# Optimization experiments

Hardware: AMD Instinct MI355X
Metric: run time of the kernel (lower is better)

The kernel has to match this reference:

```python
import jax, jax.numpy as jnp
import numpy as np

EPS = 1e-5
N_HEAD = 8
D_MODEL = 1024
D_K = D_MODEL // N_HEAD


def setup_inputs() -> dict:
    key = jax.random.key(0)
    ks = jax.random.split(key, 6)
    B, N = 4, 8192
    scale = 0.02
    return {
        "query": jax.random.normal(ks[0], (B, N, D_MODEL), jnp.float32),
        "key": jax.random.normal(ks[1], (B, N, D_MODEL), jnp.float32),
        "value": jax.random.normal(ks[2], (B, N, D_MODEL), jnp.float32),
        "Wq": jax.random.normal(ks[3], (D_MODEL, D_MODEL), jnp.float32) * scale,
        "bq": jnp.zeros((D_MODEL,), jnp.float32),
        "Wk": jax.random.normal(ks[4], (D_MODEL, D_MODEL), jnp.float32) * scale,
        "bk": jnp.zeros((D_MODEL,), jnp.float32),
        "Wv": jax.random.normal(ks[5], (D_MODEL, D_MODEL), jnp.float32) * scale,
        "bv": jnp.zeros((D_MODEL,), jnp.float32),
        "gamma_K": jnp.ones((N_HEAD, D_K), jnp.float32),
        "beta_K": jnp.zeros((N_HEAD, D_K), jnp.float32),
        "gamma_V": jnp.ones((N_HEAD, D_K), jnp.float32),
        "beta_V": jnp.zeros((N_HEAD, D_K), jnp.float32),
    }


def _proj_heads(x, W, b):
    # x: [B,N,D], torch Linear: x @ W.T + b -> [B,H,N,d_k]
    B, N, _ = x.shape
    y = jnp.einsum('bnd,ed->bne', x, W) + b
    return y.reshape(B, N, N_HEAD, D_K).transpose(0, 2, 1, 3)


def _layernorm_per_head(x, gamma, beta):
    # x: [B,H,N,d_k]; gamma/beta: [H,d_k] broadcast over batch and seq
    mu = jnp.mean(x, axis=-1, keepdims=True)
    var = jnp.mean((x - mu) ** 2, axis=-1, keepdims=True)
    xn = (x - mu) * jax.lax.rsqrt(var + EPS)
    return xn * gamma[None, :, None, :] + beta[None, :, None, :]


def reference(query, key, value, Wq, bq, Wk, bk, Wv, bv,
              gamma_K, beta_K, gamma_V, beta_V):
    B, N, _ = query.shape
    q = _proj_heads(query, Wq, bq)   # [B,H,N,dk]
    k = _proj_heads(key, Wk, bk)
    v = _proj_heads(value, Wv, bv)
    # galerkin: layernorm on K and V per head
    k = _layernorm_per_head(k, gamma_K, beta_K)
    v = _layernorm_per_head(v, gamma_V, beta_V)
    # linear attention: (K^T V)/N then Q @ (.)
    scores = jnp.einsum('bhnd,bhne->bhde', k, v)  # [B,H,dk,dk]
    p_attn = scores / N
    x = jnp.einsum('bhnd,bhde->bhne', q, p_attn)  # [B,H,N,dk]
    att_output = x.transpose(0, 2, 1, 3).reshape(B, N, N_HEAD * D_K)
    return (att_output, p_attn)
```

## Files before the change

kernel.cpp:

```cpp
#include <hip/hip_runtime.h>
#include <stdint.h>

#define DM 1024
#define NHEAD 8
#define DK 128
#define BATCH 4
#define SEQ 8192
#define ROWS (BATCH*SEQ)
#define EPSL 1e-5f
#define NSPLIT 8

typedef __attribute__((ext_vector_type(8)))  short    bf16x8;
typedef __attribute__((ext_vector_type(4)))  short    short4v;
typedef __attribute__((ext_vector_type(4)))  float    f32x4;
typedef __attribute__((ext_vector_type(4)))  float    float4v;
typedef __attribute__((ext_vector_type(2)))  uint32_t uint2v;
typedef __attribute__((ext_vector_type(4)))  uint32_t uint4v;

union AFrag { bf16x8 v; short4v h[2]; int i4[4]; };
union U8    { uint4v v[2]; uint32_t u[8]; };

__device__ inline uint32_t pack2bf(float a, float b){
  uint32_t ua = __builtin_bit_cast(uint32_t, a) + 0x8000u;
  uint32_t ub = __builtin_bit_cast(uint32_t, b) + 0x8000u;
  return (ua >> 16) | (ub & 0xffff0000u);
}

__global__ void wconv_kernel(const float* __restrict__ src, uint32_t* __restrict__ dst, int n8){
  int i = blockIdx.x*256 + threadIdx.x;
  if (i >= n8) return;
  const float4v* s = (const float4v*)src;
  float4v v0 = s[2*i], v1 = s[2*i+1];
  uint4v o;
  o.x = pack2bf(v0.x, v0.y); o.y = pack2bf(v0.z, v0.w);
  o.z = pack2bf(v1.x, v1.y); o.w = pack2bf(v1.z, v1.w);
  ((uint4v*)dst)[i] = o;
}

template<int MODE>
__global__ __launch_bounds__(256, 2)
void gemm_core(const float* __restrict__ A, const uint16_t* __restrict__ Bw,
               const float* __restrict__ bias, const float* __restrict__ gamma,
               const float* __restrict__ beta, uint16_t* __restrict__ outb,
               float* __restrict__ outf)
{
  __shared__ uint16_t As[128][36];
  __shared__ uint16_t Bs[128][36];
  __shared__ float red_s[2][128];
  __shared__ float red_q[2][128];

  const int tid = threadIdx.x;
  const int id  = blockIdx.x;
  const int xcd = id & 7, j = id >> 3;
  const int bM  = ((j >> 3) << 3) | xcd;
  const int bN  = j & 7;
  const int lane = tid & 63, wv = tid >> 6;
  const int wm = wv & 1, wn = wv >> 1;
  const int l15 = lane & 15, l4 = lane >> 4;

  const int sr = tid >> 1, sh = tid & 1;
  const float* Ap = A + (size_t)(bM*128 + sr)*DM + sh*16;
  const uint16_t* Bbase = Bw + (MODE==1 ? (size_t)(bM>>6)*1048576 : (size_t)0);
  const uint16_t* Bp = Bbase + (size_t)(bN*128 + sr)*DM + sh*16;
  uint32_t* asw = (uint32_t*)&As[sr][sh*16];
  uint32_t* bsw = (uint32_t*)&Bs[sr][sh*16];

  f32x4 acc[4][4];
  #pragma unroll
  for (int i=0;i<4;i++)
    #pragma unroll
    for (int jj=0;jj<4;jj++) acc[i][jj] = (f32x4)(0.0f);

  const uint16_t* Ard = &As[wm*64 + l15][l4*8];
  const uint16_t* Brd = &Bs[wn*64 + l15][l4*8];

  float4v a0 = *(const float4v*)(Ap);
  float4v a1 = *(const float4v*)(Ap+4);
  float4v a2 = *(const float4v*)(Ap+8);
  float4v a3 = *(const float4v*)(Ap+12);
  uint4v  b0 = *(const uint4v*)(Bp);
  uint4v  b1 = *(const uint4v*)(Bp+8);
  Ap += 32; Bp += 32;

  for (int k0 = 0; k0 < DM; k0 += 32){
    uint32_t p0 = pack2bf(a0.x,a0.y), p1 = pack2bf(a0.z,a0.w);
    uint32_t p2 = pack2bf(a1.x,a1.y), p3 = pack2bf(a1.z,a1.w);
    uint32_t p4 = pack2bf(a2.x,a2.y), p5 = pack2bf(a2.z,a2.w);
    uint32_t p6 = pack2bf(a3.x,a3.y), p7 = pack2bf(a3.z,a3.w);
    uint4v  c0 = b0, c1 = b1;
    __syncthreads();
    { uint2v t; t.x=p0;   t.y=p1;   ((uint2v*)asw)[0]=t; }
    { uint2v t; t.x=p2;   t.y=p3;   ((uint2v*)asw)[1]=t; }
    { uint2v t; t.x=p4;   t.y=p5;   ((uint2v*)asw)[2]=t; }
    { uint2v t; t.x=p6;   t.y=p7;   ((uint2v*)asw)[3]=t; }
    { uint2v t; t.x=c0.x; t.y=c0.y; ((uint2v*)bsw)[0]=t; }
    { uint2v t; t.x=c0.z; t.y=c0.w; ((uint2v*)bsw)[1]=t; }
    { uint2v t; t.x=c1.x; t.y=c1.y; ((uint2v*)bsw)[2]=t; }
    { uint2v t; t.x=c1.z; t.y=c1.w; ((uint2v*)bsw)[3]=t; }
    __syncthreads();

    if (k0 + 32 < DM){
      a0 = *(const float4v*)(Ap);
      a1 = *(const float4v*)(Ap+4);
      a2 = *(const float4v*)(Ap+8);
      a3 = *(const float4v*)(Ap+12);
      b0 = *(const uint4v*)(Bp);
      b1 = *(const uint4v*)(Bp+8);
      Ap += 32; Bp += 32;
    }

    AFrag af[4], bf4[4];
    #pragma unroll
    for (int mt=0; mt<4; mt++){
      af[mt].h[0] = *(const short4v*)(Ard + mt*16*36);
      af[mt].h[1] = *(const short4v*)(Ard + mt*16*36 + 4);
    }
    #pragma unroll
    for (int nt=0; nt<4; nt++){
      bf4[nt].h[0] = *(const short4v*)(Brd + nt*16*36);
      bf4[nt].h[1] = *(const short4v*)(Brd + nt*16*36 + 4);
    }
    #pragma unroll
    for (int mt=0; mt<4; mt++)
      #pragma unroll
      for (int nt=0; nt<4; nt++)
        acc[mt][nt] = __builtin_amdgcn_mfma_f32_16x16x32_bf16(af[mt].v, bf4[nt].v, acc[mt][nt], 0, 0, 0);
  }

  if (MODE == 0){
    float bv[4], gv[4], btv[4];
    #pragma unroll
    for (int nt=0; nt<4; nt++){
      int col = bN*128 + wn*64 + nt*16 + l15;
      bv[nt] = bias[col]; gv[nt] = gamma[col]; btv[nt] = beta[col];
    }
    #pragma unroll
    for (int mt=0; mt<4; mt++){
      #pragma unroll
      for (int i=0; i<4; i++){
        float sm = 0.f, sq = 0.f;
        #pragma unroll
        for (int nt=0; nt<4; nt++){
          float v = acc[mt][nt][i] + bv[nt];
          acc[mt][nt][i] = v;
          sm += v; sq += v*v;
        }
        #pragma unroll
        for (int off=1; off<16; off<<=1){
          sm += __shfl_xor(sm, off, 16);
          sq += __shfl_xor(sq, off, 16);
        }
        if (l15 == 0){
          int rl = wm*64 + mt*16 + l4*4 + i;
          red_s[wn][rl] = sm; red_q[wn][rl] = sq;
        }
      }
    }
    __syncthreads();
    #pragma unroll
    for (int mt=0; mt<4; mt++){
      #pragma unroll
      for (int i=0; i<4; i++){
        int rl = wm*64 + mt*16 + l4*4 + i;
        float sum = red_s[0][rl] + red_s[1][rl];
        float ssq = red_q[0][rl] + red_q[1][rl];
        float mean = sum * (1.f/DK);
        float var  = ssq * (1.f/DK) - mean*mean;
        float rs   = rsqrtf(var + EPSL);
        size_t row = (size_t)(bM*128 + rl);
        #pragma unroll
        for (int nt=0; nt<4; nt++){
          int col = bN*128 + wn*64 + nt*16 + l15;
          float o = (acc[mt][nt][i] - mean)*rs*gv[nt] + btv[nt];
          uint32_t u = __builtin_bit_cast(uint32_t, o) + 0x8000u;
          outb[row*DM + col] = (uint16_t)(u >> 16);
        }
      }
    }
  } else {
    const int bb = bM >> 6;
    float bv[4];
    #pragma unroll
    for (int nt=0; nt<4; nt++)
      bv[nt] = bias[bb*DM + bN*128 + wn*64 + nt*16 + l15];
    #pragma unroll
    for (int mt=0; mt<4; mt++){
      #pragma unroll
      for (int i=0; i<4; i++){
        size_t row = (size_t)(bM*128 + wm*64 + mt*16 + l4*4 + i);
        #pragma unroll
        for (int nt=0; nt<4; nt++){
          int col = bN*128 + wn*64 + nt*16 + l15;
          outf[row*DM + col] = acc[mt][nt][i] + bv[nt];
        }
      }
    }
  }
}

__global__ __launch_bounds__(256, 2)
void scores_kernel(const uint16_t* __restrict__ kln, const uint16_t* __restrict__ vln,
                   float* __restrict__ part)
{
  __shared__ uint16_t kT[128][70];
  __shared__ uint16_t vT[128][70];
  const int tid = threadIdx.x;
  const int sp = blockIdx.x & 7, bh = blockIdx.x >> 3;
  const int b = bh >> 3, h = bh & 7;
  const int lane = tid & 63, wv = tid >> 6, wm = wv & 1, wn = wv >> 1;
  const int l15 = lane & 15, l4 = lane >> 4;
  const int dg = tid & 7, np = tid >> 3;

  f32x4 acc[4][4];
  #pragma unroll
  for (int i=0;i<4;i++)
    #pragma unroll
    for (int jj=0;jj<4;jj++) acc[i][jj] = (f32x4)(0.0f);

  const size_t hb = (size_t)b*SEQ*DM + (size_t)h*DK;

  auto load_slab = [&](int nc, U8& k0, U8& k1, U8& v0, U8& v1){
    const int n0 = sp*1024 + nc*64;
    const uint16_t* kp = kln + hb + (size_t)(n0 + 2*np)*DM + dg*16;
    const uint16_t* vp = vln + hb + (size_t)(n0 + 2*np)*DM + dg*16;
    k0.v[0] = *(const uint4v*)(kp);       k0.v[1] = *(const uint4v*)(kp+8);
    k1.v[0] = *(const uint4v*)(kp+DM);    k1.v[1] = *(const uint4v*)(kp+DM+8);
    v0.v[0] = *(const uint4v*)(vp);       v0.v[1] = *(const uint4v*)(vp+8);
    v1.v[0] = *(const uint4v*)(vp+DM);    v1.v[1] = *(const uint4v*)(vp+DM+8);
  };

  U8 k0, k1, v0, v1;
  load_slab(0, k0, k1, v0, v1);

  for (int nc = 0; nc < 16; nc++){
    __syncthreads();
    #pragma unroll
    for (int q=0; q<8; q++){
      uint32_t ke = (k0.u[q] & 0xffffu) | (k1.u[q] << 16);
      uint32_t ko = (k0.u[q] >> 16)     | (k1.u[q] & 0xffff0000u);
      uint32_t ve = (v0.u[q] & 0xffffu) | (v1.u[q] << 16);
      uint32_t vo = (v0.u[q] >> 16)     | (v1.u[q] & 0xffff0000u);
      int d = dg*16 + q*2;
      *(uint32_t*)&kT[d  ][2*np] = ke;
      *(uint32_t*)&kT[d+1][2*np] = ko;
      *(uint32_t*)&vT[d  ][2*np] = ve;
      *(uint32_t*)&vT[d+1][2*np] = vo;
    }
    __syncthreads();

    if (nc + 1 < 16) load_slab(nc + 1, k0, k1, v0, v1);

    #pragma unroll
    for (int ks=0; ks<2; ks++){
      const int koff = ks*32 + l4*8;
      AFrag af[4], bf4[4];
      #pragma unroll
      for (int mt=0; mt<4; mt++){
        const uint16_t* pr = &kT[wm*64 + mt*16 + l15][koff];
        af[mt].i4[0] = *(const int*)(pr);
        af[mt].i4[1] = *(const int*)(pr+2);
        af[mt].i4[2] = *(const int*)(pr+4);
        af[mt].i4[3] = *(const int*)(pr+6);
      }
      #pragma unroll
      for (int nt=0; nt<4; nt++){
        const uint16_t* pr = &vT[wn*64 + nt*16 + l15][koff];
        bf4[nt].i4[0] = *(const int*)(pr);
        bf4[nt].i4[1] = *(const int*)(pr+2);
        bf4[nt].i4[2] = *(const int*)(pr+4);
        bf4[nt].i4[3] = *(const int*)(pr+6);
      }
      #pragma unroll
      for (int mt=0; mt<4; mt++)
        #pragma unroll
        for (int nt=0; nt<4; nt++)
          acc[mt][nt] = __builtin_amdgcn_mfma_f32_16x16x32_bf16(af[mt].v, bf4[nt].v, acc[mt][nt], 0, 0, 0);
    }
  }
  float* po = part + (size_t)(sp*32 + bh)*16384;
  #pragma unroll
  for (int mt=0; mt<4; mt++)
    #pragma unroll
    for (int i=0; i<4; i++){
      int d = wm*64 + mt*16 + l4*4 + i;
      #pragma unroll
      for (int nt=0; nt<4; nt++){
        int e = wn*64 + nt*16 + l15;
        po[d*128 + e] = acc[mt][nt][i];
      }
    }
}

__global__ void reduce_kernel(const float* __restrict__ part, float* __restrict__ pout){
  int i = blockIdx.x*256 + threadIdx.x;
  const float4v* p4 = (const float4v*)part;
  float4v s = p4[i];
  #pragma unroll
  for (int sp2=1; sp2<NSPLIT; sp2++) s += p4[(size_t)sp2*131072 + i];
  s *= (1.0f/(float)SEQ);
  ((float4v*)pout)[i] = s;
}

__global__ __launch_bounds__(256)
void fold_kernel(const float* __restrict__ Wq, const float* __restrict__ p,
                 uint16_t* __restrict__ WcT)
{
  const int dblk = blockIdx.x, h = blockIdx.y, b = blockIdx.z;
  const int t = threadIdx.x;
  const int eg = t & 15, dq = t >> 4;
  const int e0 = eg*8, d0 = dq*8;
  const float* pbase = p + (size_t)((b*NHEAD + h)*DK)*DK;
  const float* wbase = Wq + (size_t)h*DK*DM + dblk*128;
  float accf[8][8];
  #pragma unroll
  for (int i=0;i<8;i++)
    #pragma unroll
    for (int jj=0;jj<8;jj++) accf[i][jj] = 0.f;
  for (int f=0; f<DK; f++){
    float4v pa = *(const float4v*)(pbase + f*DK + e0);
    float4v pc = *(const float4v*)(pbase + f*DK + e0 + 4);
    float4v wa = *(const float4v*)(wbase + (size_t)f*DM + d0);
    float4v wc = *(const float4v*)(wbase + (size_t)f*DM + d0 + 4);
    float pe[8] = {pa.x,pa.y,pa.z,pa.w,pc.x,pc.y,pc.z,pc.w};
    float we[8] = {wa.x,wa.y,wa.z,wa.w,wc.x,wc.y,wc.z,wc.w};
    #pragma unroll
    for (int i=0;i<8;i++)
      #pragma unroll
      for (int jj=0;jj<8;jj++) accf[i][jj] += pe[i]*we[jj];
  }
  uint16_t* ob = WcT + (size_t)b*1048576 + (size_t)(h*DK)*DM + dblk*128;
  #pragma unroll
  for (int i=0;i<8;i++){
    uint4v ov;
    ov.x = pack2bf(accf[i][0], accf[i][1]);
    ov.y = pack2bf(accf[i][2], accf[i][3]);
    ov.z = pack2bf(accf[i][4], accf[i][5]);
    ov.w = pack2bf(accf[i][6], accf[i][7]);
    *(uint4v*)(ob + (size_t)(e0+i)*DM + d0) = ov;
  }
}

__global__ void bc_kernel(const float* __restrict__ bq, const float* __restrict__ p,
                          float* __restrict__ bc)
{
  int gid = blockIdx.x*256 + threadIdx.x;
  int b = gid >> 10, col = gid & 1023, h = col >> 7, e = col & 127;
  float s = 0.f;
  for (int f=0; f<DK; f++)
    s += bq[h*DK + f] * p[(size_t)((b*NHEAD + h)*DK + f)*DK + e];
  bc[gid] = s;
}

extern "C" void kernel_launch(void* const* d_in, const int* in_sizes, int n_in,
                              void* d_out, int out_size, void* d_ws, size_t ws_size,
                              hipStream_t stream)
{
  const float* query = (const float*)d_in[0];
  const float* key   = (const float*)d_in[1];
  const float* value = (const float*)d_in[2];
  const float* Wq    = (const float*)d_in[3];
  const float* bq    = (const float*)d_in[4];
  const float* Wk    = (const float*)d_in[5];
  const float* bk    = (const float*)d_in[6];
  const float* Wv    = (const float*)d_in[7];
  const float* bv    = (const float*)d_in[8];
  const float* gK    = (const float*)d_in[9];
  const float* bK    = (const float*)d_in[10];
  const float* gV    = (const float*)d_in[11];
  const float* bV    = (const float*)d_in[12];
  float* out = (float*)d_out;

  char* ws = (char*)d_ws;
  uint16_t* kln  = (uint16_t*)(ws);
  uint16_t* vln  = (uint16_t*)(ws + 67108864);
  uint16_t* wkb  = (uint16_t*)(ws + 134217728);
  uint16_t* wvb  = (uint16_t*)(ws + 136314880);
  float*    part = (float*)   (ws + 138412032);
  uint16_t* wct  = (uint16_t*)(ws + 155189248);
  float*    bc   = (float*)   (ws + 163577856);

  float* pout = out + 33554432;

  wconv_kernel<<<512, 256, 0, stream>>>(Wk, (uint32_t*)wkb, 131072);
  wconv_kernel<<<512, 256, 0, stream>>>(Wv, (uint32_t*)wvb, 131072);
  gemm_core<0><<<2048, 256, 0, stream>>>(key,   wkb, bk, gK, bK, kln, nullptr);
  gemm_core<0><<<2048, 256, 0, stream>>>(value, wvb, bv, gV, bV, vln, nullptr);
  scores_kernel<<<256, 256, 0, stream>>>(kln, vln, part);
  reduce_kernel<<<512, 256, 0, stream>>>(part, pout);
  fold_kernel<<<dim3(8,8,4), 256, 0, stream>>>(Wq, pout, wct);
  bc_kernel<<<16, 256, 0, stream>>>(bq, pout, bc);
  gemm_core<1><<<2048, 256, 0, stream>>>(query, wct, bc, nullptr, nullptr, nullptr, out);
}
```

Before: 879.0 us.

## Pre-convert activations to bf16 and load GEMM tiles with global_load_lds

Measured after the change: 793.2 us. -9.8%, faster.

```diff
diff --git a/kernel.cpp b/kernel.cpp
--- a/kernel.cpp
+++ b/kernel.cpp
@@ -20,13 +20,19 @@
 union AFrag { bf16x8 v; short4v h[2]; int i4[4]; };
 union U8    { uint4v v[2]; uint32_t u[8]; };
 
+typedef __attribute__((address_space(1))) const unsigned int GU32;
+typedef __attribute__((address_space(3))) unsigned int LU32;
+__device__ __forceinline__ void gload16(const void* g, void* l){
+  __builtin_amdgcn_global_load_lds((GU32*)g, (LU32*)l, 16, 0, 0);
+}
+
 __device__ inline uint32_t pack2bf(float a, float b){
   uint32_t ua = __builtin_bit_cast(uint32_t, a) + 0x8000u;
   uint32_t ub = __builtin_bit_cast(uint32_t, b) + 0x8000u;
   return (ua >> 16) | (ub & 0xffff0000u);
 }
 
-__global__ void wconv_kernel(const float* __restrict__ src, uint32_t* __restrict__ dst, int n8){
+__global__ void conv_kernel(const float* __restrict__ src, uint32_t* __restrict__ dst, int n8){
   int i = blockIdx.x*256 + threadIdx.x;
   if (i >= n8) return;
   const float4v* s = (const float4v*)src;
@@ -39,92 +45,70 @@
 
 template<int MODE>
 __global__ __launch_bounds__(256, 2)
-void gemm_core(const float* __restrict__ A, const uint16_t* __restrict__ Bw,
-               const float* __restrict__ bias, const float* __restrict__ gamma,
-               const float* __restrict__ beta, uint16_t* __restrict__ outb,
-               float* __restrict__ outf)
+void gemm_bf(const uint16_t* __restrict__ A, const uint16_t* __restrict__ Bw,
+             const float* __restrict__ bias, const float* __restrict__ gamma,
+             const float* __restrict__ beta, uint16_t* __restrict__ outb,
+             float* __restrict__ outf)
 {
-  __shared__ uint16_t As[128][36];
-  __shared__ uint16_t Bs[128][36];
+  __shared__ uint16_t As[128*64];
+  __shared__ uint16_t Bs[128*64];
   __shared__ float red_s[2][128];
   __shared__ float red_q[2][128];
 
   const int tid = threadIdx.x;
   const int id  = blockIdx.x;
-  const int xcd = id & 7, j = id >> 3;
-  const int bM  = ((j >> 3) << 3) | xcd;
-  const int bN  = j & 7;
+  const int xcd = id & 7, jj0 = id >> 3;
+  const int bM  = ((jj0 >> 3) << 3) | xcd;
+  const int bN  = jj0 & 7;
   const int lane = tid & 63, wv = tid >> 6;
   const int wm = wv & 1, wn = wv >> 1;
   const int l15 = lane & 15, l4 = lane >> 4;
 
-  const int sr = tid >> 1, sh = tid & 1;
-  const float* Ap = A + (size_t)(bM*128 + sr)*DM + sh*16;
-  const uint16_t* Bbase = Bw + (MODE==1 ? (size_t)(bM>>6)*1048576 : (size_t)0);
-  const uint16_t* Bp = Bbase + (size_t)(bN*128 + sr)*DM + sh*16;
-  uint32_t* asw = (uint32_t*)&As[sr][sh*16];
-  uint32_t* bsw = (uint32_t*)&Bs[sr][sh*16];
+  const int srow = tid >> 3;
+  const int sc   = tid & 7;
+
+  const uint16_t* Ab = A + (size_t)(bM*128)*DM;
+  const uint16_t* Bb = Bw + (MODE==1 ? (size_t)(bM>>6)*1048576 : (size_t)0)
+                          + (size_t)(bN*128)*DM;
 
   f32x4 acc[4][4];
   #pragma unroll
   for (int i=0;i<4;i++)
     #pragma unroll
-    for (int jj=0;jj<4;jj++) acc[i][jj] = (f32x4)(0.0f);
-
-  const uint16_t* Ard = &As[wm*64 + l15][l4*8];
-  const uint16_t* Brd = &Bs[wn*64 + l15][l4*8];
-
-  float4v a0 = *(const float4v*)(Ap);
-  float4v a1 = *(const float4v*)(Ap+4);
-  float4v a2 = *(const float4v*)(Ap+8);
-  float4v a3 = *(const float4v*)(Ap+12);
-  uint4v  b0 = *(const uint4v*)(Bp);
-  uint4v  b1 = *(const uint4v*)(Bp+8);
-  Ap += 32; Bp += 32;
-
-  for (int k0 = 0; k0 < DM; k0 += 32){
-    uint32_t p0 = pack2bf(a0.x,a0.y), p1 = pack2bf(a0.z,a0.w);
-    uint32_t p2 = pack2bf(a1.x,a1.y), p3 = pack2bf(a1.z,a1.w);
-    uint32_t p4 = pack2bf(a2.x,a2.y), p5 = pack2bf(a2.z,a2.w);
-    uint32_t p6 = pack2bf(a3.x,a3.y), p7 = pack2bf(a3.z,a3.w);
-    uint4v  c0 = b0, c1 = b1;
-    __syncthreads();
-    { uint2v t; t.x=p0;   t.y=p1;   ((uint2v*)asw)[0]=t; }
-    { uint2v t; t.x=p2;   t.y=p3;   ((uint2v*)asw)[1]=t; }
-    { uint2v t; t.x=p4;   t.y=p5;   ((uint2v*)asw)[2]=t; }
-    { uint2v t; t.x=p6;   t.y=p7;   ((uint2v*)asw)[3]=t; }
-    { uint2v t; t.x=c0.x; t.y=c0.y; ((uint2v*)bsw)[0]=t; }
-    { uint2v t; t.x=c0.z; t.y=c0.w; ((uint2v*)bsw)[1]=t; }
-    { uint2v t; t.x=c1.x; t.y=c1.y; ((uint2v*)bsw)[2]=t; }
-    { uint2v t; t.x=c1.z; t.y=c1.w; ((uint2v*)bsw)[3]=t; }
-    __syncthreads();
-
-    if (k0 + 32 < DM){
-      a0 = *(const float4v*)(Ap);
-      a1 = *(const float4v*)(Ap+4);
-      a2 = *(const float4v*)(Ap+8);
-      a3 = *(const float4v*)(Ap+12);
-      b0 = *(const uint4v*)(Bp);
-      b1 = *(const uint4v*)(Bp+8);
-      Ap += 32; Bp += 32;
-    }
-
-    AFrag af[4], bf4[4];
-    #pragma unroll
-    for (int mt=0; mt<4; mt++){
-      af[mt].h[0] = *(const short4v*)(Ard + mt*16*36);
-      af[mt].h[1] = *(const short4v*)(Ard + mt*16*36 + 4);
-    }
-    #pragma unroll
-    for (int nt=0; nt<4; nt++){
-      bf4[nt].h[0] = *(const short4v*)(Brd + nt*16*36);
-      bf4[nt].h[1] = *(const short4v*)(Brd + nt*16*36 + 4);
-    }
-    #pragma unroll
-    for (int mt=0; mt<4; mt++)
-      #pragma unroll
-      for (int nt=0; nt<4; nt++)
-        acc[mt][nt] = __builtin_amdgcn_mfma_f32_16x16x32_bf16(af[mt].v, bf4[nt].v, acc[mt][nt], 0, 0, 0);
+    for (int j=0;j<4;j++) acc[i][j] = (f32x4)(0.0f);
+
+  for (int k0 = 0; k0 < DM; k0 += 64){
+    __syncthreads();
+    #pragma unroll
+    for (int jr = 0; jr < 4; jr++){
+      const int row = srow + 32*jr;
+      const int g = (sc - row) & 7;
+      gload16(Ab + (size_t)row*DM + k0 + g*8, &As[row*64 + sc*8]);
+      gload16(Bb + (size_t)row*DM + k0 + g*8, &Bs[row*64 + sc*8]);
+    }
+    __syncthreads();
+
+    #pragma unroll
+    for (int ks = 0; ks < 2; ks++){
+      AFrag af[4], bf4[4];
+      #pragma unroll
+      for (int mt=0; mt<4; mt++){
+        const int r = wm*64 + mt*16 + l15;
+        const int slot = (ks*4 + l4 + r) & 7;
+        af[mt].v = *(const bf16x8*)&As[r*64 + slot*8];
+      }
+      #pragma unroll
+      for (int nt=0; nt<4; nt++){
+        const int r = wn*64 + nt*16 + l15;
+        const int slot = (ks*4 + l4 + r) & 7;
+        bf4[nt].v = *(const bf16x8*)&Bs[r*64 + slot*8];
+      }
+      #pragma unroll
+      for (int mt=0; mt<4; mt++)
+        #pragma unroll
+        for (int nt=0; nt<4; nt++)
+          acc[mt][nt] = __builtin_amdgcn_mfma_f32_16x16x32_bf16(af[mt].v, bf4[nt].v, acc[mt][nt], 0, 0, 0);
+    }
   }
 
   if (MODE == 0){
@@ -199,6 +183,144 @@
 }
 
 __global__ __launch_bounds__(256, 2)
+void gemm_fused(const float* __restrict__ A, const uint16_t* __restrict__ Bw,
+                const float* __restrict__ bias, const float* __restrict__ gamma,
+                const float* __restrict__ beta, uint16_t* __restrict__ outb)
+{
+  __shared__ uint16_t As[128][36];
+  __shared__ uint16_t Bs[128][36];
+  __shared__ float red_s[2][128];
+  __shared__ float red_q[2][128];
+
+  const int tid = threadIdx.x;
+  const int id  = blockIdx.x;
+  const int xcd = id & 7, j = id >> 3;
+  const int bM  = ((j >> 3) << 3) | xcd;
+  const int bN  = j & 7;
+  const int lane = tid & 63, wv = tid >> 6;
+  const int wm = wv & 1, wn = wv >> 1;
+  const int l15 = lane & 15, l4 = lane >> 4;
+
+  const int sr = tid >> 1, sh = tid & 1;
+  const float* Ap = A + (size_t)(bM*128 + sr)*DM + sh*16;
+  const uint16_t* Bp = Bw + (size_t)(bN*128 + sr)*DM + sh*16;
+  uint32_t* asw = (uint32_t*)&As[sr][sh*16];
+  uint32_t* bsw = (uint32_t*)&Bs[sr][sh*16];
+
+  f32x4 acc[4][4];
+  #pragma unroll
+  for (int i=0;i<4;i++)
+    #pragma unroll
+    for (int jj=0;jj<4;jj++) acc[i][jj] = (f32x4)(0.0f);
+
+  const uint16_t* Ard = &As[wm*64 + l15][l4*8];
+  const uint16_t* Brd = &Bs[wn*64 + l15][l4*8];
+
+  float4v a0 = *(const float4v*)(Ap);
+  float4v a1 = *(const float4v*)(Ap+4);
+  float4v a2 = *(const float4v*)(Ap+8);
+  float4v a3 = *(const float4v*)(Ap+12);
+  uint4v  b0 = *(const uint4v*)(Bp);
+  uint4v  b1 = *(const uint4v*)(Bp+8);
+  Ap += 32; Bp += 32;
+
+  for (int k0 = 0; k0 < DM; k0 += 32){
+    uint32_t p0 = pack2bf(a0.x,a0.y), p1 = pack2bf(a0.z,a0.w);
+    uint32_t p2 = pack2bf(a1.x,a1.y), p3 = pack2bf(a1.z,a1.w);
+    uint32_t p4 = pack2bf(a2.x,a2.y), p5 = pack2bf(a2.z,a2.w);
+    uint32_t p6 = pack2bf(a3.x,a3.y), p7 = pack2bf(a3.z,a3.w);
+    uint4v  c0 = b0, c1 = b1;
+    __syncthreads();
+    { uint2v t; t.x=p0;   t.y=p1;   ((uint2v*)asw)[0]=t; }
+    { uint2v t; t.x=p2;   t.y=p3;   ((uint2v*)asw)[1]=t; }
+    { uint2v t; t.x=p4;   t.y=p5;   ((uint2v*)asw)[2]=t; }
+    { uint2v t; t.x=p6;   t.y=p7;   ((uint2v*)asw)[3]=t; }
+    { uint2v t; t.x=c0.x; t.y=c0.y; ((uint2v*)bsw)[0]=t; }
+    { uint2v t; t.x=c0.z; t.y=c0.w; ((uint2v*)bsw)[1]=t; }
+    { uint2v t; t.x=c1.x; t.y=c1.y; ((uint2v*)bsw)[2]=t; }
+    { uint2v t; t.x=c1.z; t.y=c1.w; ((uint2v*)bsw)[3]=t; }
+    __syncthreads();
+
+    if (k0 + 32 < DM){
+      a0 = *(const float4v*)(Ap);
+      a1 = *(const float4v*)(Ap+4);
+      a2 = *(const float4v*)(Ap+8);
+      a3 = *(const float4v*)(Ap+12);
+      b0 = *(const uint4v*)(Bp);
+      b1 = *(const uint4v*)(Bp+8);
+      Ap += 32; Bp += 32;
+    }
+
+    AFrag af[4], bf4[4];
+    #pragma unroll
+    for (int mt=0; mt<4; mt++){
+      af[mt].h[0] = *(const short4v*)(Ard + mt*16*36);
+      af[mt].h[1] = *(const short4v*)(Ard + mt*16*36 + 4);
+    }
+    #pragma unroll
+    for (int nt=0; nt<4; nt++){
+      bf4[nt].h[0] = *(const short4v*)(Brd + nt*16*36);
+      bf4[nt].h[1] = *(const short4v*)(Brd + nt*16*36 + 4);
+    }
+    #pragma unroll
+    for (int mt=0; mt<4; mt++)
+      #pragma unroll
+      for (int nt=0; nt<4; nt++)
+        acc[mt][nt] = __builtin_amdgcn_mfma_f32_16x16x32_bf16(af[mt].v, bf4[nt].v, acc[mt][nt], 0, 0, 0);
+  }
+
+  float bv[4], gv[4], btv[4];
+  #pragma unroll
+  for (int nt=0; nt<4; nt++){
+    int col = bN*128 + wn*64 + nt*16 + l15;
+    bv[nt] = bias[col]; gv[nt] = gamma[col]; btv[nt] = beta[col];
+  }
+  #pragma unroll
+  for (int mt=0; mt<4; mt++){
+    #pragma unroll
+    for (int i=0; i<4; i++){
+      float sm = 0.f, sq = 0.f;
+      #pragma unroll
+      for (int nt=0; nt<4; nt++){
+        float v = acc[mt][nt][i] + bv[nt];
+        acc[mt][nt][i] = v;
+        sm += v; sq += v*v;
+      }
+      #pragma unroll
+      for (int off=1; off<16; off<<=1){
+        sm += __shfl_xor(sm, off, 16);
+        sq += __shfl_xor(sq, off, 16);
+      }
+      if (l15 == 0){
+        int rl = wm*64 + mt*16 + l4*4 + i;
+        red_s[wn][rl] = sm; red_q[wn][rl] = sq;
+      }
+    }
+  }
+  __syncthreads();
+  #pragma unroll
+  for (int mt=0; mt<4; mt++){
+    #pragma unroll
+    for (int i=0; i<4; i++){
+      int rl = wm*64 + mt*16 + l4*4 + i;
+      float sum = red_s[0][rl] + red_s[1][rl];
+      float ssq = red_q[0][rl] + red_q[1][rl];
+      float mean = sum * (1.f/DK);
+      float var  = ssq * (1.f/DK) - mean*mean;
+      float rs   = rsqrtf(var + EPSL);
+      size_t row = (size_t)(bM*128 + rl);
+      #pragma unroll
+      for (int nt=0; nt<4; nt++){
+        int col = bN*128 + wn*64 + nt*16 + l15;
+        float o = (acc[mt][nt][i] - mean)*rs*gv[nt] + btv[nt];
+        uint32_t u = __builtin_bit_cast(uint32_t, o) + 0x8000u;
+        outb[row*DM + col] = (uint16_t)(u >> 16);
+      }
+    }
+  }
+}
+
+__global__ __launch_bounds__(256, 2)
 void scores_kernel(const uint16_t* __restrict__ kln, const uint16_t* __restrict__ vln,
                    float* __restrict__ part)
 {
@@ -368,26 +490,58 @@
   const float* bK    = (const float*)d_in[10];
   const float* gV    = (const float*)d_in[11];
   const float* bV    = (const float*)d_in[12];
-  float* out = (float*)d_out;
+  float* out  = (float*)d_out;
+  float* pout = out + 33554432;
 
   char* ws = (char*)d_ws;
-  uint16_t* kln  = (uint16_t*)(ws);
-  uint16_t* vln  = (uint16_t*)(ws + 67108864);
-  uint16_t* wkb  = (uint16_t*)(ws + 134217728);
-  uint16_t* wvb  = (uint16_t*)(ws + 136314880);
-  float*    part = (float*)   (ws + 138412032);
-  uint16_t* wct  = (uint16_t*)(ws + 155189248);
-  float*    bc   = (float*)   (ws + 163577856);
-
-  float* pout = out + 33554432;
-
-  wconv_kernel<<<512, 256, 0, stream>>>(Wk, (uint32_t*)wkb, 131072);
-  wconv_kernel<<<512, 256, 0, stream>>>(Wv, (uint32_t*)wvb, 131072);
-  gemm_core<0><<<2048, 256, 0, stream>>>(key,   wkb, bk, gK, bK, kln, nullptr);
-  gemm_core<0><<<2048, 256, 0, stream>>>(value, wvb, bv, gV, bV, vln, nullptr);
-  scores_kernel<<<256, 256, 0, stream>>>(kln, vln, part);
-  reduce_kernel<<<512, 256, 0, stream>>>(part, pout);
-  fold_kernel<<<dim3(8,8,4), 256, 0, stream>>>(Wq, pout, wct);
-  bc_kernel<<<16, 256, 0, stream>>>(bq, pout, bc);
-  gemm_core<1><<<2048, 256, 0, stream>>>(query, wct, bc, nullptr, nullptr, nullptr, out);
-}
+  const int N8_ACT = 4194304;
+  const int N8_W   = 131072;
+
+  if (ws_size >= (size_t)364920832ull){
+    uint16_t* kln = (uint16_t*)(ws);
+    uint16_t* vln = (uint16_t*)(ws + 67108864);
+    uint16_t* qbf = (uint16_t*)(ws + 134217728);
+    uint16_t* kbf = (uint16_t*)(ws + 201326592);
+    uint16_t* vbf = (uint16_t*)(ws + 268435456);
+    uint16_t* wkb = (uint16_t*)(ws + 335544320);
+    uint16_t* wvb = (uint16_t*)(ws + 337641472);
+    float*    part= (float*)   (ws + 339738624);
+    uint16_t* wct = (uint16_t*)(ws + 356515840);
+    float*    bc  = (float*)   (ws + 364904448);
+
+    conv_kernel<<<16384, 256, 0, stream>>>(key,   (uint32_t*)kbf, N8_ACT);
+    conv_kernel<<<16384, 256, 0, stream>>>(value, (uint32_t*)vbf, N8_ACT);
+    conv_kernel<<<16384, 256, 0, stream>>>(query, (uint32_t*)qbf, N8_ACT);
+    conv_kernel<<<512,   256, 0, stream>>>(Wk,    (uint32_t*)wkb, N8_W);
+    conv_kernel<<<512,   256, 0, stream>>>(Wv,    (uint32_t*)wvb, N8_W);
+    gemm_bf<0><<<2048, 256, 0, stream>>>(kbf, wkb, bk, gK, bK, kln, nullptr);
+    gemm_bf<0><<<2048, 256, 0, stream>>>(vbf, wvb, bv, gV, bV, vln, nullptr);
+    scores_kernel<<<256, 256, 0, stream>>>(kln, vln, part);
+    reduce_kernel<<<512, 256, 0, stream>>>(part, pout);
+    fold_kernel<<<dim3(8,8,4), 256, 0, stream>>>(Wq, pout, wct);
+    bc_kernel<<<16, 256, 0, stream>>>(bq, pout, bc);
+    gemm_bf<1><<<2048, 256, 0, stream>>>(qbf, wct, bc, nullptr, nullptr, nullptr, out);
+  } else {
+    uint16_t* kbf = (uint16_t*)(ws);
+    uint16_t* vln = (uint16_t*)(ws);
+    uint16_t* wct = (uint16_t*)(ws);
+    float*    bc  = (float*)   (ws + 8388608);
+    uint16_t* kln = (uint16_t*)(ws + 67108864);
+    uint16_t* qbf = (uint16_t*)(ws + 67108864);
+    uint16_t* wkb = (uint16_t*)(ws + 134217728);
+    uint16_t* wvb = (uint16_t*)(ws + 136314880);
+    float*    part= (float*)   (d_out);
+
+    conv_kernel<<<512,   256, 0, stream>>>(Wk,  (uint32_t*)wkb, N8_W);
+    conv_kernel<<<512,   256, 0, stream>>>(Wv,  (uint32_t*)wvb, N8_W);
+    conv_kernel<<<16384, 256, 0, stream>>>(key, (uint32_t*)kbf, N8_ACT);
+    gemm_bf<0><<<2048, 256, 0, stream>>>(kbf, wkb, bk, gK, bK, kln, nullptr);
+    gemm_fused<<<2048, 256, 0, stream>>>(value, wvb, bv, gV, bV, vln);
+    scores_kernel<<<256, 256, 0, stream>>>(kln, vln, part);
+    reduce_kernel<<<512, 256, 0, stream>>>(part, pout);
+    conv_kernel<<<16384, 256, 0, stream>>>(query, (uint32_t*)qbf, N8_ACT);
+    fold_kernel<<<dim3(8,8,4), 256, 0, stream>>>(Wq, pout, wct);
+    bc_kernel<<<16, 256, 0, stream>>>(bq, pout, bc);
+    gemm_bf<1><<<2048, 256, 0, stream>>>(qbf, wct, bc, nullptr, nullptr, nullptr, out);
+  }
+}
```
